# Kernel optimization log

Measured on AMD Instinct MI355X. Metric: run time of the kernel, lower is better.

## Reference

```python
import jax, jax.numpy as jnp
import numpy as np

SEQ_LEN = 256
HIDDEN = 1024
OUT = 512
BATCH = 256


def setup_inputs() -> dict:
    key = jax.random.key(0)
    ks = jax.random.split(key, 7)
    s_h = 1.0 / np.sqrt(HIDDEN)
    c_vector = jax.random.normal(ks[0], (BATCH, HIDDEN), dtype=jnp.float32)
    # PyTorch LSTMCell params: weight_ih (4H, I), weight_hh (4H, H), biases (4H)
    W_ih = jax.random.uniform(ks[1], (4 * HIDDEN, OUT), jnp.float32, -s_h, s_h)
    W_hh = jax.random.uniform(ks[2], (4 * HIDDEN, HIDDEN), jnp.float32, -s_h, s_h)
    b_ih = jax.random.uniform(ks[3], (4 * HIDDEN,), jnp.float32, -s_h, s_h)
    b_hh = jax.random.uniform(ks[4], (4 * HIDDEN,), jnp.float32, -s_h, s_h)
    W_out = jax.random.uniform(ks[5], (OUT, HIDDEN), jnp.float32, -s_h, s_h)
    b_out = jax.random.uniform(ks[6], (OUT,), jnp.float32, -s_h, s_h)
    return {"c_vector": c_vector, "W_ih": W_ih, "W_hh": W_hh, "b_ih": b_ih,
            "b_hh": b_hh, "W_out": W_out, "b_out": b_out}


def reference(c_vector, W_ih, W_hh, b_ih, b_hh, W_out, b_out):
    B = c_vector.shape[0]
    bias = b_ih + b_hh

    def step(carry, _):
        h, c, x = carry
        gates = x @ W_ih.T + h @ W_hh.T + bias  # (B, 4H)
        i, f, g, o = jnp.split(gates, 4, axis=-1)  # PyTorch gate order i,f,g,o
        c_new = jax.nn.sigmoid(f) * c + jax.nn.sigmoid(i) * jnp.tanh(g)
        h_new = jax.nn.sigmoid(o) * jnp.tanh(c_new)
        o_t = c_new @ W_out.T + b_out  # fc_out applied to cell state, per source
        return (h_new, c_new, o_t), (h_new, c_new, o_t)

    x0 = jnp.zeros((B, W_ih.shape[1]), dtype=c_vector.dtype)
    _, (hs, cs, outs) = jax.lax.scan(step, (c_vector, c_vector, x0), None, length=SEQ_LEN)
    # scan stacks on axis 0 (time); source returns (B, T, .)
    return (jnp.swapaxes(hs, 0, 1), jnp.swapaxes(cs, 0, 1), jnp.swapaxes(outs, 0, 1))
```

## Files before the change

kernel.cpp:

```cpp
#include <hip/hip_runtime.h>
#include <cstdint>
#include <cstddef>
#include <type_traits>


#define SEQ    256
#define BATCH  256
#define HID    1024
#define OUTD   512
#define KDIM   2048
#define GATES  4096

typedef __bf16 bf16x8 __attribute__((ext_vector_type(8)));
typedef float  f32x4  __attribute__((ext_vector_type(4)));

__device__ __forceinline__ unsigned short f2bf(float x) {
  unsigned u = __float_as_uint(x);
  u = (u + 0x7FFFu + ((u >> 16) & 1u)) >> 16;
  return (unsigned short)u;
}

__device__ __forceinline__ f32x4 mfma16(bf16x8 a, bf16x8 b, f32x4 c) {
  return __builtin_amdgcn_mfma_f32_16x16x32_bf16(a, b, c, 0, 0, 0);
}

__device__ __forceinline__ bf16x8 ld_frag_bf(const unsigned short* p) {
  uint4 u = *reinterpret_cast<const uint4*>(p);
  return __builtin_bit_cast(bf16x8, u);
}

__device__ __forceinline__ float rcp_fast(float x) {
  float r;
  asm("v_rcp_f32 %0, %1" : "=v"(r) : "v"(x));
  return r;
}
__device__ __forceinline__ float sigmoid_fast(float x) {
  return rcp_fast(1.f + __expf(-x));
}
__device__ __forceinline__ float tanh_fast(float x) {
  float xc = fminf(fmaxf(x, -15.f), 15.f);
  float e2 = __expf(2.f * xc);
  return 1.f - 2.f * rcp_fast(1.f + e2);
}

#define GLOAD_LDS16(gp, lp)                                                   \
  __builtin_amdgcn_global_load_lds(                                           \
      (const __attribute__((address_space(1))) unsigned int*)(gp),            \
      (__attribute__((address_space(3))) unsigned int*)(lp), 16, 0, 0)


__global__ void k_cast_whh(const float* __restrict__ whh, unsigned short* __restrict__ wg2) {
  int i4 = blockIdx.x * blockDim.x + threadIdx.x;
  if (i4 >= (GATES * HID) / 4) return;
  int idx = i4 * 4;
  int n = idx >> 10, k = idx & 1023;
  const float4 v = *reinterpret_cast<const float4*>(whh + idx);
  ushort4 o; o.x = f2bf(v.x); o.y = f2bf(v.y); o.z = f2bf(v.z); o.w = f2bf(v.w);
  *reinterpret_cast<ushort4*>(wg2 + (size_t)n * KDIM + k) = o;
}

__global__ void k_cast_wout(const float* __restrict__ wout,
                            unsigned short* __restrict__ wott) {
  int idx = blockIdx.x * blockDim.x + threadIdx.x;
  if (idx >= OUTD * HID) return;
  int j = idx >> 10, k = idx & 1023;
  wott[(size_t)k * OUTD + j] = f2bf(wout[idx]);
}

__global__ void k_init(const float* __restrict__ cvec,
                       unsigned short* __restrict__ a0,
                       unsigned* __restrict__ flags) {
  int idx = blockIdx.x * blockDim.x + threadIdx.x;
  if (idx < 256) flags[idx] = 0u;
  if (idx >= BATCH * KDIM) return;
  int b = idx >> 11, k = idx & 2047;
  a0[idx] = (k < HID) ? f2bf(cvec[(size_t)b * HID + k]) : (unsigned short)0;
}

__global__ void k_bias(const float* __restrict__ wih, const float* __restrict__ b_ih,
                       const float* __restrict__ b_hh, const float* __restrict__ b_out,
                       float* __restrict__ bias0, float* __restrict__ bias2) {
  int wave = threadIdx.x >> 6, l = threadIdx.x & 63;
  int n = blockIdx.x * 4 + wave;
  float s = 0.f;
  for (int j = l; j < OUTD; j += 64) s += wih[(size_t)n * OUTD + j] * b_out[j];
  for (int off = 32; off; off >>= 1) s += __shfl_down(s, off);
  if (l == 0) {
    float b0 = b_ih[n] + b_hh[n];
    bias0[n] = b0;
    bias2[n] = b0 + s;
  }
}

template <typename AT>
__device__ __forceinline__ bf16x8 ld_frag(const AT* p) {
  if constexpr (std::is_same_v<AT, float>) {
    const float4 f0 = *reinterpret_cast<const float4*>(p);
    const float4 f1 = *reinterpret_cast<const float4*>(p + 4);
    uint4 v;
    v.x = (unsigned)f2bf(f0.x) | ((unsigned)f2bf(f0.y) << 16);
    v.y = (unsigned)f2bf(f0.z) | ((unsigned)f2bf(f0.w) << 16);
    v.z = (unsigned)f2bf(f1.x) | ((unsigned)f2bf(f1.y) << 16);
    v.w = (unsigned)f2bf(f1.z) | ((unsigned)f2bf(f1.w) << 16);
    return __builtin_bit_cast(bf16x8, v);
  } else {
    return ld_frag_bf(p);
  }
}

template <typename AT, typename BT, typename DT>
__global__ __launch_bounds__(256)
void k_gemm(const AT* __restrict__ A, int lda,
            const BT* __restrict__ Bn, int ldb,
            DT* __restrict__ D, int ldd,
            const float* __restrict__ bias, int K) {
  __shared__ char lds[64 * 1024];
  const int tid = threadIdx.x;
  const int w = tid >> 6, l = tid & 63;
  const int n0 = blockIdx.x * 64;
  const int m0 = blockIdx.y * 64 + w * 16;
  const int lr = l & 15, lg = l >> 4;

  f32x4 acc[4] = {};
  for (int kc = 0; kc < K; kc += 512) {
    __syncthreads();
    for (int it = 0; it < 16; ++it) {
      int idx = tid + it * 256;
      int col = idx >> 6, k16 = idx & 63;
      uint4 v;
      if constexpr (std::is_same_v<BT, float>) {
        const float* src = Bn + (size_t)(n0 + col) * ldb + kc + k16 * 8;
        const float4 f0 = *reinterpret_cast<const float4*>(src);
        const float4 f1 = *reinterpret_cast<const float4*>(src + 4);
        v.x = (unsigned)f2bf(f0.x) | ((unsigned)f2bf(f0.y) << 16);
        v.y = (unsigned)f2bf(f0.z) | ((unsigned)f2bf(f0.w) << 16);
        v.z = (unsigned)f2bf(f1.x) | ((unsigned)f2bf(f1.y) << 16);
        v.w = (unsigned)f2bf(f1.z) | ((unsigned)f2bf(f1.w) << 16);
      } else {
        v = *reinterpret_cast<const uint4*>(Bn + (size_t)(n0 + col) * ldb + kc + k16 * 8);
      }
      int db = col * 1024 + ((k16 * 16) ^ ((col & 7) << 4));
      *reinterpret_cast<uint4*>(lds + db) = v;
    }
    __syncthreads();
    const AT* Arow = A + (size_t)(m0 + lr) * lda + kc + lg * 8;
#pragma unroll
    for (int ks = 0; ks < 16; ++ks) {
      bf16x8 af = ld_frag(Arow + ks * 32);
      int kb = ks * 64 + lg * 16;
#pragma unroll
      for (int f = 0; f < 4; ++f) {
        int col = f * 16 + lr;
        uint4 u = *reinterpret_cast<const uint4*>(lds + col * 1024 + (kb ^ ((col & 7) << 4)));
        acc[f] = mfma16(af, __builtin_bit_cast(bf16x8, u), acc[f]);
      }
    }
  }
#pragma unroll
  for (int f = 0; f < 4; ++f) {
    int cg = n0 + f * 16 + lr;
    float bv = bias ? bias[cg] : 0.f;
#pragma unroll
    for (int j = 0; j < 4; ++j) {
      int r = m0 + lg * 4 + j;
      float val = acc[f][j] + bv;
      if constexpr (std::is_same_v<DT, unsigned short>) D[(size_t)r * ldd + cg] = f2bf(val);
      else                                              D[(size_t)r * ldd + cg] = val;
    }
  }
}

__global__ __launch_bounds__(512, 2)
void k_lstm_p3(unsigned short* __restrict__ Ab0,
               unsigned short* __restrict__ Ab1,
               const unsigned short* __restrict__ Wg2,
               const float* __restrict__ bias0,
               const float* __restrict__ bias2,
               const float* __restrict__ cvec,
               float* __restrict__ hs,
               float* __restrict__ cs,
               unsigned* __restrict__ flags) {
  __shared__ char lds[131072];
  const int tid = threadIdx.x;
  const int wave = tid >> 6, l = tid & 63;
  const int wn = wave >> 2, wk = wave & 3;
  const int bid = blockIdx.x;
  const int mg = (bid & 7) >> 1;
  const int ng = (bid >> 3) | ((bid & 1) << 5);
  const int lr = l & 15, lg = l >> 4;

  bf16x8 B[8][2][2];
#pragma unroll
  for (int c = 0; c < 8; ++c)
#pragma unroll
    for (int ks = 0; ks < 2; ++ks)
#pragma unroll
      for (int in = 0; in < 2; ++in) {
        int col = wn * 32 + in * 16 + lr;
        int grow = (col >> 4) * HID + ng * 16 + (col & 15);
        int kb = c * 256 + wk * 64 + ks * 32 + lg * 8;
        B[c][ks][in] = ld_frag_bf(Wg2 + (size_t)grow * KDIM + kb);
      }

  const int m = tid >> 3;
  const int hcp = tid & 7;
  const int b_row = mg * 64 + m;
  const int hid0 = ng * 16 + hcp * 2;
  float creg[2];
  {
    const float2 cv = *reinterpret_cast<const float2*>(cvec + (size_t)b_row * HID + hid0);
    creg[0] = cv.x; creg[1] = cv.y;
  }
  float b0r[2][4], b2r[2][4];
#pragma unroll
  for (int e = 0; e < 2; ++e)
#pragma unroll
    for (int g = 0; g < 4; ++g) {
      b0r[e][g] = bias0[g * HID + hid0 + e];
      b2r[e][g] = bias2[g * HID + hid0 + e];
    }
  asm volatile("s_waitcnt vmcnt(0)" ::: "memory");

  for (int t = 0; t < SEQ; ++t) {
    const unsigned short* Acur = (t & 1) ? Ab1 : Ab0;
    unsigned short* Anxt = (t & 1) ? Ab0 : Ab1;

    if (t > 0) {
      if (wave == 0) {
        for (;;) {
          unsigned v = __hip_atomic_load(&flags[(mg << 6) + l],
                                         __ATOMIC_RELAXED, __HIP_MEMORY_SCOPE_AGENT);
          if (__all((int)(v >= (unsigned)t))) break;
          __builtin_amdgcn_s_sleep(0);
        }
        (void)__hip_atomic_load(&flags[mg << 6], __ATOMIC_ACQUIRE,
                                __HIP_MEMORY_SCOPE_AGENT);
      }
      __syncthreads();
    }

    auto STAGE = [&](int buf, int c) {
      const unsigned short* base = Acur + (size_t)(mg * 64) * KDIM + c * 256;
#pragma unroll
      for (int it = 0; it < 4; ++it) {
        int s_lin = it * 512 + tid;
        int row = s_lin >> 5, slot = s_lin & 31;
        const unsigned short* g = base + (size_t)row * KDIM + ((slot ^ (row & 7)) * 8);
        GLOAD_LDS16(g, lds + buf * 32768 + s_lin * 16);
      }
    };

    STAGE(0, 0);
    STAGE(1, 1);
    STAGE(2, 2);

    f32x4 acc[4][2] = {};
#pragma unroll
    for (int c = 0; c < 8; ++c) {
      if (c <= 5)      { asm volatile("s_waitcnt vmcnt(8)" ::: "memory"); }
      else if (c == 6) { asm volatile("s_waitcnt vmcnt(4)" ::: "memory"); }
      else             { asm volatile("s_waitcnt vmcnt(0)" ::: "memory"); }
      __builtin_amdgcn_s_barrier();
      const char* buf = lds + (c & 3) * 32768;
#pragma unroll
      for (int ks = 0; ks < 2; ++ks) {
        bf16x8 a[4];
#pragma unroll
        for (int im = 0; im < 4; ++im) {
          int row = im * 16 + lr;
          int k16 = wk * 8 + ks * 4 + lg;
          a[im] = *reinterpret_cast<const bf16x8*>(
              buf + row * 512 + ((k16 ^ (row & 7)) << 4));
        }
#pragma unroll
        for (int im = 0; im < 4; ++im)
#pragma unroll
          for (int in = 0; in < 2; ++in)
            acc[im][in] = mfma16(a[im], B[c][ks][in], acc[im][in]);
      }
      if (c <= 4) STAGE((c + 3) & 3, c + 3);
    }

    asm volatile("" ::: "memory");
    __builtin_amdgcn_s_barrier();
#pragma unroll
    for (int im = 0; im < 4; ++im)
#pragma unroll
      for (int in = 0; in < 2; ++in)
        *reinterpret_cast<f32x4*>(lds + wave * 8192 + (im * 2 + in) * 1024 + l * 16) =
            acc[im][in];
    __syncthreads();

    float cn2[2], hn2[2];
#pragma unroll
    for (int e = 0; e < 2; ++e) {
      int hc = hcp * 2 + e;
      float pre[4];
#pragma unroll
      for (int g = 0; g < 4; ++g) {
        int n = g * 16 + hc;
        int wn_r = n >> 5, nn = n & 31;
        int frag = ((m >> 4) << 1) | (nn >> 4);
        int lane_r = ((m & 15) >> 2) * 16 + (nn & 15);
        int j = m & 3;
        float s = 0.f;
#pragma unroll
        for (int wkk = 0; wkk < 4; ++wkk)
          s += *reinterpret_cast<const float*>(
              lds + (wn_r * 4 + wkk) * 8192 + frag * 1024 + lane_r * 16 + j * 4);
        pre[g] = s + ((t == 0) ? b0r[e][g] : b2r[e][g]);
      }
      float si = sigmoid_fast(pre[0]);
      float sf = sigmoid_fast(pre[1]);
      float so = sigmoid_fast(pre[3]);
      float tg = tanh_fast(pre[2]);
      float cn = sf * creg[e] + si * tg;
      float hn = so * tanh_fast(cn);
      creg[e] = cn;
      cn2[e] = cn;
      hn2[e] = hn;
    }
    unsigned hpack = (unsigned)f2bf(hn2[0]) | ((unsigned)f2bf(hn2[1]) << 16);
    unsigned cpack = (unsigned)f2bf(cn2[0]) | ((unsigned)f2bf(cn2[1]) << 16);
    __hip_atomic_store(reinterpret_cast<unsigned*>(Anxt + (size_t)b_row * KDIM + hid0),
                       hpack, __ATOMIC_RELAXED, __HIP_MEMORY_SCOPE_AGENT);
    __hip_atomic_store(reinterpret_cast<unsigned*>(Anxt + (size_t)b_row * KDIM + HID + hid0),
                       cpack, __ATOMIC_RELAXED, __HIP_MEMORY_SCOPE_AGENT);
    asm volatile("s_waitcnt vmcnt(0)" ::: "memory");
    __builtin_amdgcn_s_barrier();
    if (tid == 0)
      __hip_atomic_store(&flags[(mg << 6) + ng], (unsigned)(t + 1),
                         __ATOMIC_RELAXED, __HIP_MEMORY_SCOPE_AGENT);
    size_t o = (size_t)b_row * (SEQ * HID) + (size_t)t * HID + hid0;
    *reinterpret_cast<float2*>(hs + o) = make_float2(hn2[0], hn2[1]);
    *reinterpret_cast<float2*>(cs + o) = make_float2(cn2[0], cn2[1]);
  }
}

extern "C" void kernel_launch(void* const* d_in, const int* in_sizes, int n_in,
                              void* d_out, int out_size, void* d_ws, size_t ws_size,
                              hipStream_t stream) {
  const float* c_vec = (const float*)d_in[0];
  const float* W_ih  = (const float*)d_in[1];
  const float* W_hh  = (const float*)d_in[2];
  const float* b_ih  = (const float*)d_in[3];
  const float* b_hh  = (const float*)d_in[4];
  const float* W_out = (const float*)d_in[5];
  const float* b_out = (const float*)d_in[6];

  float* out = (float*)d_out;
  float* hs = out;
  float* cs = out + (size_t)BATCH * SEQ * HID;
  float* os = out + (size_t)2 * BATCH * SEQ * HID;

  char* sc = (char*)os;
  unsigned short* Wg2   = (unsigned short*)(sc);
  unsigned short* WoTT  = (unsigned short*)(sc + (16u << 20));
  unsigned short* A0    = (unsigned short*)(sc + (17u << 20));
  unsigned short* A1    = (unsigned short*)(sc + (18u << 20));
  float*          bias0 = (float*)(sc + (19u << 20));
  float*          bias2 = (float*)(sc + (19u << 20) + 16384);
  unsigned*       g_flg = (unsigned*)(sc + (19u << 20) + 32768);

  k_cast_whh<<<dim3(GATES * HID / 4 / 256), dim3(256), 0, stream>>>(W_hh, Wg2);
  k_cast_wout<<<dim3(OUTD * HID / 256), dim3(256), 0, stream>>>(W_out, WoTT);
  k_init<<<dim3(BATCH * KDIM / 256), dim3(256), 0, stream>>>(c_vec, A0, g_flg);
  k_bias<<<dim3(GATES / 4), dim3(256), 0, stream>>>(W_ih, b_ih, b_hh, b_out, bias0, bias2);
  k_gemm<float, unsigned short, unsigned short>
      <<<dim3(HID / 64, GATES / 64), dim3(256), 0, stream>>>(
      W_ih, OUTD, WoTT, OUTD, Wg2 + HID, KDIM, (const float*)nullptr, OUTD);

  {
    void* args[] = {(void*)&A0, (void*)&A1, (void*)&Wg2, (void*)&bias0,
                    (void*)&bias2, (void*)&c_vec, (void*)&hs, (void*)&cs,
                    (void*)&g_flg};
    hipLaunchCooperativeKernel((const void*)k_lstm_p3, dim3(256), dim3(512),
                               args, 0, stream);
  }

  k_gemm<float, float, float>
      <<<dim3(OUTD / 64, BATCH * SEQ / 64), dim3(256), 0, stream>>>(
      cs, HID, W_out, HID, os, OUTD, b_out, HID);
}
```

Before: 2.830 ms.

## Replace LDS-staged A tiles with direct register loads and full-K wave split

The persistent LSTM kernel no longer stages the recurrent input tile through LDS with async global-to-LDS loads and barriers. Each of the 8 waves now owns a 256-wide K slice across all 64 output columns and loads its A fragments directly from global memory into registers, double-buffering them. The cross-wave reduction grows from 4 partials to 8. This removes the per-chunk barriers and LDS staging traffic on the serial critical path, at the cost of uncoalesced global fragment loads, a larger LDS reduction, and more accumulator registers.

Measured after the change: 4.018 ms. 1.42x slower.

```diff
diff --git a/kernel.cpp b/kernel.cpp
--- a/kernel.cpp
+++ b/kernel.cpp
@@ -42,11 +42,6 @@
   float e2 = __expf(2.f * xc);
   return 1.f - 2.f * rcp_fast(1.f + e2);
 }
-
-#define GLOAD_LDS16(gp, lp)                                                   \
-  __builtin_amdgcn_global_load_lds(                                           \
-      (const __attribute__((address_space(1))) unsigned int*)(gp),            \
-      (__attribute__((address_space(3))) unsigned int*)(lp), 16, 0, 0)
 
 
 __global__ void k_cast_whh(const float* __restrict__ whh, unsigned short* __restrict__ wg2) {
@@ -171,7 +166,7 @@
 }
 
 __global__ __launch_bounds__(512, 2)
-void k_lstm_p3(unsigned short* __restrict__ Ab0,
+void k_lstm_p4(unsigned short* __restrict__ Ab0,
                unsigned short* __restrict__ Ab1,
                const unsigned short* __restrict__ Wg2,
                const float* __restrict__ bias0,
@@ -183,24 +178,18 @@
   __shared__ char lds[131072];
   const int tid = threadIdx.x;
   const int wave = tid >> 6, l = tid & 63;
-  const int wn = wave >> 2, wk = wave & 3;
   const int bid = blockIdx.x;
   const int mg = (bid & 7) >> 1;
   const int ng = (bid >> 3) | ((bid & 1) << 5);
   const int lr = l & 15, lg = l >> 4;
 
-  bf16x8 B[8][2][2];
-#pragma unroll
-  for (int c = 0; c < 8; ++c)
-#pragma unroll
-    for (int ks = 0; ks < 2; ++ks)
-#pragma unroll
-      for (int in = 0; in < 2; ++in) {
-        int col = wn * 32 + in * 16 + lr;
-        int grow = (col >> 4) * HID + ng * 16 + (col & 15);
-        int kb = c * 256 + wk * 64 + ks * 32 + lg * 8;
-        B[c][ks][in] = ld_frag_bf(Wg2 + (size_t)grow * KDIM + kb);
-      }
+  bf16x8 B[8][4];
+#pragma unroll
+  for (int ks = 0; ks < 8; ++ks)
+#pragma unroll
+    for (int in = 0; in < 4; ++in)
+      B[ks][in] = ld_frag_bf(Wg2 + (size_t)(in * HID + ng * 16 + lr) * KDIM
+                             + wave * 256 + ks * 32 + lg * 8);
 
   const int m = tid >> 3;
   const int hcp = tid & 7;
@@ -219,7 +208,6 @@
       b0r[e][g] = bias0[g * HID + hid0 + e];
       b2r[e][g] = bias2[g * HID + hid0 + e];
     }
-  asm volatile("s_waitcnt vmcnt(0)" ::: "memory");
 
   for (int t = 0; t < SEQ; ++t) {
     const unsigned short* Acur = (t & 1) ? Ab1 : Ab0;
@@ -239,55 +227,38 @@
       __syncthreads();
     }
 
-    auto STAGE = [&](int buf, int c) {
-      const unsigned short* base = Acur + (size_t)(mg * 64) * KDIM + c * 256;
-#pragma unroll
-      for (int it = 0; it < 4; ++it) {
-        int s_lin = it * 512 + tid;
-        int row = s_lin >> 5, slot = s_lin & 31;
-        const unsigned short* g = base + (size_t)row * KDIM + ((slot ^ (row & 7)) * 8);
-        GLOAD_LDS16(g, lds + buf * 32768 + s_lin * 16);
-      }
-    };
-
-    STAGE(0, 0);
-    STAGE(1, 1);
-    STAGE(2, 2);
-
-    f32x4 acc[4][2] = {};
-#pragma unroll
-    for (int c = 0; c < 8; ++c) {
-      if (c <= 5)      { asm volatile("s_waitcnt vmcnt(8)" ::: "memory"); }
-      else if (c == 6) { asm volatile("s_waitcnt vmcnt(4)" ::: "memory"); }
-      else             { asm volatile("s_waitcnt vmcnt(0)" ::: "memory"); }
-      __builtin_amdgcn_s_barrier();
-      const char* buf = lds + (c & 3) * 32768;
-#pragma unroll
-      for (int ks = 0; ks < 2; ++ks) {
-        bf16x8 a[4];
+    const unsigned short* Arow =
+        Acur + (size_t)(mg * 64 + lr) * KDIM + wave * 256 + lg * 8;
+    bf16x8 a0[4], a1[4];
+#pragma unroll
+    for (int im = 0; im < 4; ++im) a0[im] = ld_frag_bf(Arow + im * 16 * KDIM);
+#pragma unroll
+    for (int im = 0; im < 4; ++im) a1[im] = ld_frag_bf(Arow + im * 16 * KDIM + 32);
+
+    f32x4 acc[4][4] = {};
+#pragma unroll
+    for (int ks = 0; ks < 8; ++ks) {
+#pragma unroll
+      for (int im = 0; im < 4; ++im) {
+        bf16x8 af = (ks & 1) ? a1[im] : a0[im];
+#pragma unroll
+        for (int in = 0; in < 4; ++in)
+          acc[im][in] = mfma16(af, B[ks][in], acc[im][in]);
+      }
+      if (ks < 6) {
 #pragma unroll
         for (int im = 0; im < 4; ++im) {
-          int row = im * 16 + lr;
-          int k16 = wk * 8 + ks * 4 + lg;
-          a[im] = *reinterpret_cast<const bf16x8*>(
-              buf + row * 512 + ((k16 ^ (row & 7)) << 4));
+          bf16x8 nf = ld_frag_bf(Arow + im * 16 * KDIM + (ks + 2) * 32);
+          if (ks & 1) a1[im] = nf; else a0[im] = nf;
         }
-#pragma unroll
-        for (int im = 0; im < 4; ++im)
-#pragma unroll
-          for (int in = 0; in < 2; ++in)
-            acc[im][in] = mfma16(a[im], B[c][ks][in], acc[im][in]);
-      }
-      if (c <= 4) STAGE((c + 3) & 3, c + 3);
-    }
-
-    asm volatile("" ::: "memory");
-    __builtin_amdgcn_s_barrier();
+      }
+    }
+
 #pragma unroll
     for (int im = 0; im < 4; ++im)
 #pragma unroll
-      for (int in = 0; in < 2; ++in)
-        *reinterpret_cast<f32x4*>(lds + wave * 8192 + (im * 2 + in) * 1024 + l * 16) =
+      for (int in = 0; in < 4; ++in)
+        *reinterpret_cast<f32x4*>(lds + wave * 16384 + (im * 4 + in) * 1024 + l * 16) =
             acc[im][in];
     __syncthreads();
 
@@ -298,16 +269,12 @@
       float pre[4];
 #pragma unroll
       for (int g = 0; g < 4; ++g) {
-        int n = g * 16 + hc;
-        int wn_r = n >> 5, nn = n & 31;
-        int frag = ((m >> 4) << 1) | (nn >> 4);
-        int lane_r = ((m & 15) >> 2) * 16 + (nn & 15);
-        int j = m & 3;
+        int boff = (((m >> 4) << 2) + g) * 1024
+                 + ((((m & 15) >> 2) << 4) + hc) * 16 + ((m & 3) << 2);
         float s = 0.f;
 #pragma unroll
-        for (int wkk = 0; wkk < 4; ++wkk)
-          s += *reinterpret_cast<const float*>(
-              lds + (wn_r * 4 + wkk) * 8192 + frag * 1024 + lane_r * 16 + j * 4);
+        for (int w8 = 0; w8 < 8; ++w8)
+          s += *reinterpret_cast<const float*>(lds + w8 * 16384 + boff);
         pre[g] = s + ((t == 0) ? b0r[e][g] : b2r[e][g]);
       }
       float si = sigmoid_fast(pre[0]);
@@ -374,7 +341,7 @@
     void* args[] = {(void*)&A0, (void*)&A1, (void*)&Wg2, (void*)&bias0,
                     (void*)&bias2, (void*)&c_vec, (void*)&hs, (void*)&cs,
                     (void*)&g_flg};
-    hipLaunchCooperativeKernel((const void*)k_lstm_p3, dim3(256), dim3(512),
+    hipLaunchCooperativeKernel((const void*)k_lstm_p4, dim3(256), dim3(512),
                                args, 0, stream);
   }
 
```
